# Kernel optimization log

Measured on AMD Instinct MI355X. Metric: run time of the kernel, lower is better.

The kernel has to match this reference:

```python
import jax, jax.numpy as jnp
import numpy as np

# Conv config (matches init_kwargs)
STRIDE = (1, 1)
PADDING = ((1, 1), (1, 1))
B, CIN, COUT, H, W = 16, 128, 256, 56, 56
KH, KW = 3, 3


def _conv(x, w):
    # NCHW input, OIHW kernel, zeros padding mode
    return jax.lax.conv_general_dilated(
        x, w, window_strides=STRIDE, padding=PADDING,
        dimension_numbers=("NCHW", "OIHW", "NCHW"))


def setup_inputs() -> dict:
    key = jax.random.key(0)
    ks = jax.random.split(key, 6)
    x = jax.random.normal(ks[0], (B, CIN, H, W), dtype=jnp.float32)
    # quantized weight: integer-valued floats (output of module.Q.quantize)
    weight = jnp.round(jax.random.normal(ks[1], (COUT, CIN, KH, KW), dtype=jnp.float32) * 4.0)
    act_s = jnp.asarray(0.0625, dtype=jnp.float32)   # exp2(log_act_s)
    act_q = jnp.asarray(16.0, dtype=jnp.float32)     # exp2(log_act_q)
    azp = jnp.asarray(-4.0, dtype=jnp.float32)       # rounded act zero point (scaled by guard_a)
    wzp = jnp.round(jax.random.normal(ks[2], (COUT,), dtype=jnp.float32) * 2.0)
    fp_scale = (jax.random.uniform(ks[3], (1, COUT, 1, 1), dtype=jnp.float32) + 0.5) * 1e-3
    # bias_full has spatial extent [1, COUT, H_out, W_out]
    bias = jax.random.normal(ks[4], (1, COUT, H, W), dtype=jnp.float32) * 0.1
    guard_a = jnp.asarray(2.0, dtype=jnp.float32)    # 2**act_guard_bit
    guard_w = jnp.asarray(2.0, dtype=jnp.float32)    # 2**weight_guard_bit
    return {"x": x, "weight": weight, "act_s": act_s, "act_q": act_q,
            "azp": azp, "wzp": wzp, "fp_scale": fp_scale, "bias": bias,
            "guard_a": guard_a, "guard_w": guard_w}


def reference(x, weight, act_s, act_q, azp, wzp, fp_scale, bias, guard_a, guard_w):
    # 1) Activation quantization: clamp to quant range then round to integer grid.
    zp = azp * act_s / guard_a
    xq = jnp.clip(x, zp, zp + act_q - act_s)
    xq = guard_a * jnp.round((xq - zp) / act_s)
    # 2) Main integer conv with quantized weights.
    c1 = _conv(xq, weight)
    # 3) Ones-kernel conv: output is identical across all COUT channels,
    #    so compute once as channel-sum followed by a single-channel box conv.
    s = jnp.sum(xq, axis=1, keepdims=True)  # [B, 1, H, W]
    ones_k = jnp.ones((1, 1) + weight.shape[2:], dtype=x.dtype)
    c2 = _conv(s, ones_k)  # [B, 1, H_out, W_out], broadcasts over channels
    # 4) Affine dequant + spatially-varying bias epilogue.
    out = guard_w * c1 + wzp[None, :, None, None] * c2
    return out * fp_scale + bias
```

## Files before the change

kernel.cpp:

```cpp
#include <hip/hip_runtime.h>

#define B_    16
#define CIN_  128
#define COUT_ 256
#define H_    56
#define W_    56
#define YP    58
#define XP    64

typedef int   i32x4 __attribute__((ext_vector_type(4)));
typedef float f4    __attribute__((ext_vector_type(4)));

__device__ __forceinline__ void gload16(const void* g, void* l) {
    __builtin_amdgcn_global_load_lds(
        (const __attribute__((address_space(1))) unsigned int*)g,
        (__attribute__((address_space(3))) unsigned int*)l,
        16, 0, 0);
}

__global__ __launch_bounds__(256) void k_prep(
    const float* __restrict__ x, const float* __restrict__ w,
    const float* __restrict__ p_act_s, const float* __restrict__ p_act_q,
    const float* __restrict__ p_azp,  const float* __restrict__ p_guard_a,
    signed char* __restrict__ xqU, signed char* __restrict__ wt,
    float* __restrict__ s_pad, float* __restrict__ Wsum)
{
    int t = threadIdx.x;
    int blk = blockIdx.x;

    if (blk < 928) {
        int b = blk / YP, y = blk - b * YP;
        __shared__ signed char shq[W_ * 144];
        signed char* orow = xqU + (size_t)blk * XP * CIN_;

        if (y == 0 || y == YP - 1) {
            i32x4 pv = {(int)0x80808080, (int)0x80808080,
                        (int)0x80808080, (int)0x80808080};
            *(i32x4*)(orow + t * 32)      = pv;
            *(i32x4*)(orow + t * 32 + 16) = pv;
            if (t < XP) s_pad[(size_t)blk * XP + t] = 0.0f;
            return;
        }
        int h = y - 1;
        float act_s = p_act_s[0], act_q = p_act_q[0];
        float azp = p_azp[0], ga = p_guard_a[0];
        float zp = azp * act_s / ga;
        float hi = zp + act_q - act_s;
        float inv_s = 1.0f / act_s;

        for (int i = 0; i < 7; ++i) {
            int e = i * 256 + t;
            int cin = e / 14;
            int w4 = (e - cin * 14) * 4;
            f4 v = *(const f4*)(x + (((size_t)b * CIN_ + cin) * H_ + h) * W_ + w4);
            #pragma unroll
            for (int j = 0; j < 4; ++j) {
                float vv = fminf(fmaxf(v[j], zp), hi);
                float r = rintf((vv - zp) * inv_s);
                float uq = rintf(ga * r * 0.5f) - 128.0f;
                shq[(w4 + j) * 144 + cin] = (signed char)(int)uq;
            }
        }
        __syncthreads();
        #pragma unroll
        for (int i = 0; i < 2; ++i) {
            int T = i * 256 + t;
            int xx = T >> 3;
            int c16 = T & 7;
            union { i32x4 v; signed char c[16]; } u;
            if (xx >= 1 && xx <= W_) {
                u.v = *(const i32x4*)(shq + (xx - 1) * 144 + c16 * 16);
            } else {
                u.v = (i32x4){(int)0x80808080, (int)0x80808080,
                              (int)0x80808080, (int)0x80808080};
            }
            *(i32x4*)(orow + (size_t)xx * CIN_ + c16 * 16) = u.v;
            int sum = 0;
            #pragma unroll
            for (int j = 0; j < 16; ++j) sum += (int)u.c[j];
            sum += __shfl_xor(sum, 1);
            sum += __shfl_xor(sum, 2);
            sum += __shfl_xor(sum, 4);
            if (c16 == 0)
                s_pad[(size_t)blk * XP + xx] = (float)(2 * sum + 32768);
        }
        return;
    }

    if (blk < 1216) {
        int o = ((blk - 928) * 256 + t) * 4;
        int i_  = o >> 14;
        int cc  = (i_ >= 9) ? 1 : 0;
        int g   = i_ - cc * 9;
        int cbp = (o >> 13) & 1;
        int mh  = (o >> 12) & 1;
        int mi  = (o >> 10) & 3;
        int ln  = (o >> 4) & 63;
        int cout = cbp * 128 + mh * 64 + mi * 16 + (ln & 15);
        int cin0 = cc * 64 + (ln >> 4) * 16 + (o & 15);
        int dy = g / 3, dx = g - dy * 3;
        const float* src = w + (size_t)cout * 1152 + cin0 * 9 + dy * 3 + dx;
        union { int v; signed char c[4]; } pk;
        #pragma unroll
        for (int j = 0; j < 4; ++j)
            pk.c[j] = (signed char)(int)src[j * 9];
        *(int*)(wt + o) = pk.v;
        return;
    }

    {
        int bw = blk - 1216;
        int cout = bw * 16 + (t >> 4);
        int part = t & 15;
        const float* base = w + (size_t)cout * 1152 + part * 72;
        float s = 0.f;
        for (int j = 0; j < 72; ++j) s += base[j];
        s += __shfl_xor(s, 1);
        s += __shfl_xor(s, 2);
        s += __shfl_xor(s, 4);
        s += __shfl_xor(s, 8);
        if (part == 0) Wsum[cout] = s;
        return;
    }
}

__global__ __launch_bounds__(256, 3) void k_gemm(
    const signed char* __restrict__ xqU,
    const signed char* __restrict__ wt,
    const float* __restrict__ s_pad,
    const float* __restrict__ Wsum,
    const float* __restrict__ wzp,
    const float* __restrict__ fps,
    const float* __restrict__ bias,
    const float* __restrict__ p_gw,
    float* __restrict__ out)
{
    __shared__ __align__(16) signed char Bh[2 * 16384 + 128];
    __shared__ __align__(16) float c2s[2 * 56];

    int tid = threadIdx.x;
    int wv = tid >> 6, lane = tid & 63;
    int xl = lane & 15, q = lane >> 4;
    int bid = blockIdx.x;
    int u = (bid & 7) * 112 + (bid >> 3);
    int cb = u & 1;
    int p = u >> 1;
    int b = p / 28, hp = p - b * 28;
    int h = hp * 2;
    int mh = wv >> 1;
    int rn = wv & 1;

    if (tid < 112) {
        int rr = tid / 56, wp = tid - rr * 56;
        const float* sp = s_pad + ((size_t)(b * YP + h + rr)) * XP + wp;
        float a = 0.f;
        #pragma unroll
        for (int dy = 0; dy < 3; ++dy)
            #pragma unroll
            for (int dx = 0; dx < 3; ++dx)
                a += sp[dy * XP + dx];
        c2s[tid] = a;
    }

    const signed char* xb = xqU + (size_t)(b * YP + h) * XP * CIN_;
    #pragma unroll
    for (int cc = 0; cc < 2; ++cc)
        #pragma unroll
        for (int r_ = 0; r_ < 4; ++r_) {
            int T_ = r_ * 256 + tid;
            int p_ = T_ & 3;
            int x_ = (T_ >> 2) & 63;
            int yy_ = T_ >> 8;
            int pe_ = p_ ^ ((x_ >> 1) & 3);
            gload16(xb + (size_t)(yy_ * XP + x_) * CIN_ + cc * 64 + pe_ * 16,
                    Bh + cc * 16384 + (r_ * 256 + wv * 64) * 16);
        }

    i32x4 acc[4][4];
    #pragma unroll
    for (int mi = 0; mi < 4; ++mi)
        #pragma unroll
        for (int ni = 0; ni < 4; ++ni)
            acc[mi][ni] = (i32x4){0, 0, 0, 0};

    const signed char* aptr = wt + (size_t)(cb * 8192 + mh * 4096) + (size_t)lane * 16;
    int bn_row[4];
    #pragma unroll
    for (int ni = 0; ni < 4; ++ni)
        bn_row[ni] = rn * 4096 + (ni * 16 + xl) * 64;
    int cxo[3];
    #pragma unroll
    for (int d = 0; d < 3; ++d)
        cxo[d] = (q ^ (((d + xl) >> 1) & 3)) * 16;

    i32x4 af[2][4], bf[2][4];

    #define LDA(bufv, iv)                                                      \
        {                                                                      \
            _Pragma("unroll")                                                  \
            for (int mi_ = 0; mi_ < 4; ++mi_)                                  \
                af[bufv][mi_] = *(const i32x4*)(aptr + (iv) * 16384 + mi_ * 1024); \
        }
    #define LDB(bufv, iv)                                                      \
        {                                                                      \
            const int cc_ = ((iv) >= 9) ? 1 : 0;                               \
            const int g_ = (iv) - cc_ * 9;                                     \
            const int dy_ = g_ / 3, dx_ = g_ - dy_ * 3;                        \
            const int off_ = cc_ * 16384 + dy_ * 4096 + dx_ * 64 + cxo[dx_];   \
            _Pragma("unroll")                                                  \
            for (int ni_ = 0; ni_ < 4; ++ni_)                                  \
                bf[bufv][ni_] = *(const i32x4*)(Bh + off_ + bn_row[ni_]);      \
        }

    LDA(0, 0)
    __syncthreads();
    LDB(0, 0)

    #pragma unroll
    for (int i = 0; i < 18; ++i) {
        const int cur = i & 1, nxt = cur ^ 1;
        if (i < 17) {
            LDA(nxt, i + 1)
            LDB(nxt, i + 1)
        }
        #pragma unroll
        for (int mi = 0; mi < 4; ++mi)
            #pragma unroll
            for (int ni = 0; ni < 4; ++ni)
                acc[mi][ni] = __builtin_amdgcn_mfma_i32_16x16x64_i8(
                    bf[cur][ni], af[cur][mi], acc[mi][ni], 0, 0, 0);
    }

    #undef LDA
    #undef LDB

    float gw = p_gw[0];
    int hrow = h + rn;
    #pragma unroll
    for (int mi = 0; mi < 4; ++mi) {
        int cout = cb * 128 + mh * 64 + mi * 16 + xl;
        float wz = wzp[cout], fs = fps[cout];
        float base_c = 256.0f * Wsum[cout];
        const float* brow = bias + ((size_t)cout * H_ + hrow) * W_;
        float* orow = out + (((size_t)b * COUT_ + cout) * H_ + hrow) * W_;
        #pragma unroll
        for (int ni = 0; ni < 4; ++ni) {
            int w4 = ni * 16 + q * 4;
            if (w4 < W_) {
                f4 bi  = *(const f4*)(brow + w4);
                f4 c2v = *(const f4*)(c2s + rn * 56 + w4);
                f4 o;
                #pragma unroll
                for (int j = 0; j < 4; ++j) {
                    float c1 = 2.0f * (float)acc[mi][ni][j] + base_c;
                    o[j] = (gw * c1 + wz * c2v[j]) * fs + bi[j];
                }
                *(f4*)(orow + w4) = o;
            }
        }
    }
}

extern "C" void kernel_launch(void* const* d_in, const int* in_sizes, int n_in,
                              void* d_out, int out_size, void* d_ws, size_t ws_size,
                              hipStream_t stream)
{
    const float* x     = (const float*)d_in[0];
    const float* wht   = (const float*)d_in[1];
    const float* act_s = (const float*)d_in[2];
    const float* act_q = (const float*)d_in[3];
    const float* azp   = (const float*)d_in[4];
    const float* wzp   = (const float*)d_in[5];
    const float* fps   = (const float*)d_in[6];
    const float* bias  = (const float*)d_in[7];
    const float* ga    = (const float*)d_in[8];
    const float* gw    = (const float*)d_in[9];
    float* out = (float*)d_out;

    char* ws = (char*)d_ws;
    signed char* xqU  = (signed char*)(ws);
    signed char* wt   = (signed char*)(ws + 7602176);
    float*       spad = (float*)(ws + 7602176 + 294912);
    float*       Wsum = (float*)(ws + 7602176 + 294912 + 237568);

    k_prep<<<dim3(1232), dim3(256), 0, stream>>>(
        x, wht, act_s, act_q, azp, ga, xqU, wt, spad, Wsum);
    k_gemm<<<dim3(896), dim3(256), 0, stream>>>(
        xqU, wt, spad, Wsum, wzp, fps, bias, gw, out);
}
```

Measured before the change: 139.9 us.

## Compute four output rows per block to reuse weight fragments across two row tiles

Each GEMM block now covers four output rows instead of two. It loads a 6-row input halo into LDS and keeps two accumulator sets, so every weight (A) fragment loaded from global memory feeds twice as many MFMAs. The grid is halved to 448 blocks and launch bounds drop to 2 waves per SIMD to make room for the doubled accumulators. B fragments are no longer double-buffered, and there are fewer blocks than before on a 256-CU part, which risks poorer occupancy and load balance.

```diff
diff --git a/kernel.cpp b/kernel.cpp
--- a/kernel.cpp
+++ b/kernel.cpp
@@ -124,7 +124,7 @@
     }
 }
 
-__global__ __launch_bounds__(256, 3) void k_gemm(
+__global__ __launch_bounds__(256, 2) void k_gemm(
     const signed char* __restrict__ xqU,
     const signed char* __restrict__ wt,
     const float* __restrict__ s_pad,
@@ -135,24 +135,24 @@
     const float* __restrict__ p_gw,
     float* __restrict__ out)
 {
-    __shared__ __align__(16) signed char Bh[2 * 16384 + 128];
-    __shared__ __align__(16) float c2s[2 * 56];
+    __shared__ __align__(16) signed char Bh[2 * 6 * 4096 + 128];
+    __shared__ __align__(16) float c2s[4 * 56];
 
     int tid = threadIdx.x;
     int wv = tid >> 6, lane = tid & 63;
     int xl = lane & 15, q = lane >> 4;
     int bid = blockIdx.x;
-    int u = (bid & 7) * 112 + (bid >> 3);
+    int u = (bid & 7) * 56 + (bid >> 3);
     int cb = u & 1;
-    int p = u >> 1;
-    int b = p / 28, hp = p - b * 28;
-    int h = hp * 2;
+    int g4 = u >> 1;
+    int b = g4 / 14, hp4 = g4 - b * 14;
+    int H0 = hp4 * 4;
     int mh = wv >> 1;
     int rn = wv & 1;
 
-    if (tid < 112) {
+    if (tid < 224) {
         int rr = tid / 56, wp = tid - rr * 56;
-        const float* sp = s_pad + ((size_t)(b * YP + h + rr)) * XP + wp;
+        const float* sp = s_pad + ((size_t)(b * YP + H0 + rr)) * XP + wp;
         float a = 0.f;
         #pragma unroll
         for (int dy = 0; dy < 3; ++dy)
@@ -162,38 +162,40 @@
         c2s[tid] = a;
     }
 
-    const signed char* xb = xqU + (size_t)(b * YP + h) * XP * CIN_;
+    const signed char* xb = xqU + (size_t)(b * YP + H0) * XP * CIN_;
     #pragma unroll
     for (int cc = 0; cc < 2; ++cc)
         #pragma unroll
-        for (int r_ = 0; r_ < 4; ++r_) {
+        for (int r_ = 0; r_ < 6; ++r_) {
             int T_ = r_ * 256 + tid;
             int p_ = T_ & 3;
             int x_ = (T_ >> 2) & 63;
-            int yy_ = T_ >> 8;
+            int row_ = T_ >> 8;
             int pe_ = p_ ^ ((x_ >> 1) & 3);
-            gload16(xb + (size_t)(yy_ * XP + x_) * CIN_ + cc * 64 + pe_ * 16,
-                    Bh + cc * 16384 + (r_ * 256 + wv * 64) * 16);
-        }
-
-    i32x4 acc[4][4];
-    #pragma unroll
-    for (int mi = 0; mi < 4; ++mi)
-        #pragma unroll
-        for (int ni = 0; ni < 4; ++ni)
-            acc[mi][ni] = (i32x4){0, 0, 0, 0};
+            gload16(xb + (size_t)(row_ * XP + x_) * CIN_ + cc * 64 + pe_ * 16,
+                    Bh + cc * 24576 + (r_ * 256 + wv * 64) * 16);
+        }
+
+    i32x4 acc[2][4][4];
+    #pragma unroll
+    for (int tt = 0; tt < 2; ++tt)
+        #pragma unroll
+        for (int mi = 0; mi < 4; ++mi)
+            #pragma unroll
+            for (int ni = 0; ni < 4; ++ni)
+                acc[tt][mi][ni] = (i32x4){0, 0, 0, 0};
 
     const signed char* aptr = wt + (size_t)(cb * 8192 + mh * 4096) + (size_t)lane * 16;
-    int bn_row[4];
+    int bn_x[4];
     #pragma unroll
     for (int ni = 0; ni < 4; ++ni)
-        bn_row[ni] = rn * 4096 + (ni * 16 + xl) * 64;
+        bn_x[ni] = (ni * 16 + xl) * 64;
     int cxo[3];
     #pragma unroll
     for (int d = 0; d < 3; ++d)
         cxo[d] = (q ^ (((d + xl) >> 1) & 3)) * 16;
 
-    i32x4 af[2][4], bf[2][4];
+    i32x4 af[2][4], bf0[4], bf1[4];
 
     #define LDA(bufv, iv)                                                      \
         {                                                                      \
@@ -201,61 +203,72 @@
             for (int mi_ = 0; mi_ < 4; ++mi_)                                  \
                 af[bufv][mi_] = *(const i32x4*)(aptr + (iv) * 16384 + mi_ * 1024); \
         }
-    #define LDB(bufv, iv)                                                      \
+    #define LDB(dstv, tv, iv)                                                  \
         {                                                                      \
             const int cc_ = ((iv) >= 9) ? 1 : 0;                               \
             const int g_ = (iv) - cc_ * 9;                                     \
             const int dy_ = g_ / 3, dx_ = g_ - dy_ * 3;                        \
-            const int off_ = cc_ * 16384 + dy_ * 4096 + dx_ * 64 + cxo[dx_];   \
+            const int off_ = cc_ * 24576 + ((tv) * 2 * 4096) + dy_ * 4096      \
+                             + dx_ * 64 + cxo[dx_];                            \
+            const int roff_ = rn * 4096;                                       \
             _Pragma("unroll")                                                  \
             for (int ni_ = 0; ni_ < 4; ++ni_)                                  \
-                bf[bufv][ni_] = *(const i32x4*)(Bh + off_ + bn_row[ni_]);      \
+                dstv[ni_] = *(const i32x4*)(Bh + off_ + roff_ + bn_x[ni_]);    \
         }
 
     LDA(0, 0)
     __syncthreads();
-    LDB(0, 0)
 
     #pragma unroll
     for (int i = 0; i < 18; ++i) {
         const int cur = i & 1, nxt = cur ^ 1;
         if (i < 17) {
             LDA(nxt, i + 1)
-            LDB(nxt, i + 1)
-        }
+        }
+        LDB(bf0, 0, i)
+        LDB(bf1, 1, i)
         #pragma unroll
         for (int mi = 0; mi < 4; ++mi)
             #pragma unroll
             for (int ni = 0; ni < 4; ++ni)
-                acc[mi][ni] = __builtin_amdgcn_mfma_i32_16x16x64_i8(
-                    bf[cur][ni], af[cur][mi], acc[mi][ni], 0, 0, 0);
+                acc[0][mi][ni] = __builtin_amdgcn_mfma_i32_16x16x64_i8(
+                    bf0[ni], af[cur][mi], acc[0][mi][ni], 0, 0, 0);
+        #pragma unroll
+        for (int mi = 0; mi < 4; ++mi)
+            #pragma unroll
+            for (int ni = 0; ni < 4; ++ni)
+                acc[1][mi][ni] = __builtin_amdgcn_mfma_i32_16x16x64_i8(
+                    bf1[ni], af[cur][mi], acc[1][mi][ni], 0, 0, 0);
     }
 
     #undef LDA
     #undef LDB
 
     float gw = p_gw[0];
-    int hrow = h + rn;
-    #pragma unroll
-    for (int mi = 0; mi < 4; ++mi) {
-        int cout = cb * 128 + mh * 64 + mi * 16 + xl;
-        float wz = wzp[cout], fs = fps[cout];
-        float base_c = 256.0f * Wsum[cout];
-        const float* brow = bias + ((size_t)cout * H_ + hrow) * W_;
-        float* orow = out + (((size_t)b * COUT_ + cout) * H_ + hrow) * W_;
-        #pragma unroll
-        for (int ni = 0; ni < 4; ++ni) {
-            int w4 = ni * 16 + q * 4;
-            if (w4 < W_) {
-                f4 bi  = *(const f4*)(brow + w4);
-                f4 c2v = *(const f4*)(c2s + rn * 56 + w4);
-                f4 o;
-                #pragma unroll
-                for (int j = 0; j < 4; ++j) {
-                    float c1 = 2.0f * (float)acc[mi][ni][j] + base_c;
-                    o[j] = (gw * c1 + wz * c2v[j]) * fs + bi[j];
+    #pragma unroll
+    for (int tt = 0; tt < 2; ++tt) {
+        int hrow = H0 + tt * 2 + rn;
+        #pragma unroll
+        for (int mi = 0; mi < 4; ++mi) {
+            int cout = cb * 128 + mh * 64 + mi * 16 + xl;
+            float wz = wzp[cout], fs = fps[cout];
+            float base_c = 256.0f * Wsum[cout];
+            const float* brow = bias + ((size_t)cout * H_ + hrow) * W_;
+            float* orow = out + (((size_t)b * COUT_ + cout) * H_ + hrow) * W_;
+            #pragma unroll
+            for (int ni = 0; ni < 4; ++ni) {
+                int w4 = ni * 16 + q * 4;
+                if (w4 < W_) {
+                    f4 bi  = *(const f4*)(brow + w4);
+                    f4 c2v = *(const f4*)(c2s + (tt * 2 + rn) * 56 + w4);
+                    f4 o;
+                    #pragma unroll
+                    for (int j = 0; j < 4; ++j) {
+                        float c1 = 2.0f * (float)acc[tt][mi][ni][j] + base_c;
+                        o[j] = (gw * c1 + wz * c2v[j]) * fs + bi[j];
+                    }
+                    *(f4*)(orow + w4) = o;
                 }
-                *(f4*)(orow + w4) = o;
             }
         }
     }
@@ -285,6 +298,6 @@
 
     k_prep<<<dim3(1232), dim3(256), 0, stream>>>(
         x, wht, act_s, act_q, azp, ga, xqU, wt, spad, Wsum);
-    k_gemm<<<dim3(896), dim3(256), 0, stream>>>(
+    k_gemm<<<dim3(448), dim3(256), 0, stream>>>(
         xqU, wt, spad, Wsum, wzp, fps, bias, gw, out);
 }
```

Measured after the change: 129.6 us (median of 2 runs). -7.3%, faster.
